# Kernel tuning notes

Measured on AMD Instinct MI355X. Metric: run time of the kernel, lower is better.

## Reference

```python
import jax, jax.numpy as jnp
import numpy as np

NUM_HEAD = 16
MASKED_BIAS = -10000.0


def setup_inputs() -> dict:
    key = jax.random.key(0)
    k1, k2, k3 = jax.random.split(key, 3)
    B, M, N = 2, 2048, 1024
    x = jax.random.normal(k1, (B, M, N), dtype=jnp.float32)
    w_attn = jax.random.normal(k2, (N, 3 * N), dtype=jnp.float32) * 0.02
    w_proj = jax.random.normal(k3, (N, N), dtype=jnp.float32) * 0.02
    b_attn = jnp.zeros((3 * N,), dtype=jnp.float32)
    b_proj = jnp.zeros((N,), dtype=jnp.float32)
    return {"x": x, "w_attn": w_attn, "w_proj": w_proj,
            "b_attn": b_attn, "b_proj": b_proj}


def reference(x, w_attn, w_proj, b_attn, b_proj):
    B, M, N = x.shape
    H = NUM_HEAD
    d = N // H  # head dim
    # fused QKV projection: [B,M,3N]
    qkv = jnp.einsum('bmn,nd->bmd', x, w_attn) + b_attn
    q, k, v = jnp.split(qkv, 3, axis=-1)
    # split heads -> [B,H,M,d]
    q = q.reshape(B, M, H, d).transpose(0, 2, 1, 3)
    k = k.reshape(B, M, H, d).transpose(0, 2, 1, 3)
    v = v.reshape(B, M, H, d).transpose(0, 2, 1, 3)
    # scaled dot-product scores [B,H,M,M]
    scores = jnp.einsum('bhqd,bhkd->bhqk', q, k) / jnp.sqrt(jnp.float32(d))
    causal = jnp.tril(jnp.ones((M, M), dtype=bool))  # GPT-2 bias buffer
    scores = jnp.where(causal, scores, jnp.float32(MASKED_BIAS))
    attn = jax.nn.softmax(scores, axis=-1)
    # context [B,H,M,d] -> [B,M,N]
    ctx = jnp.einsum('bhqk,bhkd->bhqd', attn, v)
    ctx = ctx.transpose(0, 2, 1, 3).reshape(B, M, N)
    # output projection
    out = jnp.einsum('bmn,no->bmo', ctx, w_proj) + b_proj
    return out
```

## Files before the change

### kernel.cpp

```cpp
#include <hip/hip_runtime.h>

typedef __attribute__((ext_vector_type(8))) __bf16 bf16x8;
typedef __attribute__((ext_vector_type(4))) __bf16 bf16x4;
typedef __attribute__((ext_vector_type(4))) float f32x4;
typedef __attribute__((ext_vector_type(4))) short short4v;

__device__ __forceinline__ void async_copy16(const void* g, void* l) {
    __builtin_amdgcn_global_load_lds(
        (const __attribute__((address_space(1))) void*)g,
        (__attribute__((address_space(3))) void*)l, 16, 0, 0);
}

__global__ __launch_bounds__(256) void prep_k(
    const float* __restrict__ x, __bf16* __restrict__ xb,
    const float* __restrict__ wa, __bf16* __restrict__ wAt,
    const float* __restrict__ wp, __bf16* __restrict__ wPt)
{
    __shared__ float tile[32][33];
    const int bx = blockIdx.x;
    if (bx < 2048) {
        size_t i = ((size_t)bx * 256 + threadIdx.x) * 8;
        float4 a = *(const float4*)&x[i];
        float4 b = *(const float4*)&x[i + 4];
        bf16x8 o;
        o[0] = (__bf16)a.x; o[1] = (__bf16)a.y; o[2] = (__bf16)a.z; o[3] = (__bf16)a.w;
        o[4] = (__bf16)b.x; o[5] = (__bf16)b.y; o[6] = (__bf16)b.z; o[7] = (__bf16)b.w;
        *(bf16x8*)&xb[i] = o;
        return;
    }
    const float* src; __bf16* dst; int R, C, c0, r0;
    if (bx < 5120) {
        int id = bx - 2048;
        src = wa; dst = wAt; R = 1024; C = 3072;
        c0 = (id % 96) * 32; r0 = (id / 96) * 32;
    } else {
        int id = bx - 5120;
        src = wp; dst = wPt; R = 1024; C = 1024;
        c0 = (id & 31) * 32; r0 = (id >> 5) * 32;
    }
    int tx = threadIdx.x & 31, ty = threadIdx.x >> 5;
    for (int i = ty; i < 32; i += 8)
        tile[i][tx] = src[(size_t)(r0 + i) * C + (c0 + tx)];
    __syncthreads();
    for (int i = ty; i < 32; i += 8)
        dst[(size_t)(c0 + i) * R + (r0 + tx)] = (__bf16)tile[tx][i];
}

template <int MODE, int TN>
__global__ __launch_bounds__(256) void gemm_bt(
    const __bf16* __restrict__ A, const __bf16* __restrict__ Bt,
    const float* __restrict__ bias, int K,
    __bf16* __restrict__ O0, __bf16* __restrict__ O1, __bf16* __restrict__ O2,
    float* __restrict__ Of)
{
    constexpr int NJ = TN / 32;
    __shared__ __align__(16) __bf16 lds_a[128 * 32];
    __shared__ __align__(16) __bf16 lds_b[TN * 32];
    const int row0 = blockIdx.x * 128;
    const int col0 = blockIdx.y * TN;
    const int tid  = threadIdx.x;
    const int lane = tid & 63;
    const int w    = tid >> 6;
    const int wm   = (w >> 1) * 64, wn = (w & 1) * (TN / 2);
    const int quad = lane >> 4, l16 = lane & 15;

    f32x4 acc[4][NJ] = {};
    for (int kb = 0; kb < K; kb += 32) {
#pragma unroll
        for (int t = 0; t < 2; ++t) {
            int s = t * 256 + tid;
            int L = s >> 3, c = (s & 7) ^ (L & 7);
            int row = 2 * L + (c >> 2), ch = c & 3;
            async_copy16(&A[(size_t)(row0 + row) * K + kb + ch * 8],
                         (char*)lds_a + (t * 256 + w * 64) * 16);
        }
#pragma unroll
        for (int t = 0; t < TN / 64; ++t) {
            int s = t * 256 + tid;
            int L = s >> 3, c = (s & 7) ^ (L & 7);
            int row = 2 * L + (c >> 2), ch = c & 3;
            async_copy16(&Bt[(size_t)(col0 + row) * K + kb + ch * 8],
                         (char*)lds_b + (t * 256 + w * 64) * 16);
        }
        __syncthreads();
        bf16x8 af[4], bfr[NJ];
#pragma unroll
        for (int i = 0; i < 4; ++i) {
            int r = wm + i * 16 + l16;
            int L = r >> 1, g = ((r & 1) * 4 + quad) ^ (L & 7);
            af[i] = *(const bf16x8*)&lds_a[L * 64 + g * 8];
        }
#pragma unroll
        for (int j = 0; j < NJ; ++j) {
            int r = wn + j * 16 + l16;
            int L = r >> 1, g = ((r & 1) * 4 + quad) ^ (L & 7);
            bfr[j] = *(const bf16x8*)&lds_b[L * 64 + g * 8];
        }
#pragma unroll
        for (int i = 0; i < 4; ++i)
#pragma unroll
            for (int j = 0; j < NJ; ++j)
                acc[i][j] = __builtin_amdgcn_mfma_f32_16x16x32_bf16(
                    af[i], bfr[j], acc[i][j], 0, 0, 0);
        __syncthreads();
    }

#pragma unroll
    for (int i = 0; i < 4; ++i) {
        int grow = row0 + wm + i * 16 + quad * 4;
#pragma unroll
        for (int j = 0; j < NJ; ++j) {
            int gcol = col0 + wn + j * 16 + l16;
            float bv = bias[gcol];
            if constexpr (MODE == 0) {
                int which = gcol >> 10;
                int n  = gcol & 1023;
                int hh = n >> 6, dd = n & 63;
                int bb = grow >> 11, mm0 = grow & 2047;
                int bhh = bb * 16 + hh;
                if (which == 2) {
                    int w64 = mm0 & 63;
                    int mi = (mm0 & ~63) | (w64 & 32) | ((w64 & 12) << 1)
                             | ((w64 & 16) >> 2);
                    bf16x4 pk;
#pragma unroll
                    for (int r = 0; r < 4; ++r)
                        pk[r] = (__bf16)(acc[i][j][r] + bv);
                    *(bf16x4*)&O2[((size_t)bhh * 64 + dd) * 2048 + mi] = pk;
                } else {
#pragma unroll
                    for (int r = 0; r < 4; ++r) {
                        float v = acc[i][j][r] + bv;
                        if (which == 0)
                            O0[((size_t)bhh * 2048 + mm0 + r) * 64 + dd] =
                                (__bf16)(v * 0.18033688011112042f);
                        else
                            O1[((size_t)bhh * 2048 + mm0 + r) * 64 + dd] =
                                (__bf16)v;
                    }
                }
            } else {
#pragma unroll
                for (int r = 0; r < 4; ++r) {
                    int gr = grow + r;
                    Of[(size_t)gr * 1024 + gcol] = acc[i][j][r] + bv;
                }
            }
        }
    }
}

__global__ __launch_bounds__(256) void attn_kernel(
    const __bf16* __restrict__ Qh, const __bf16* __restrict__ Kh,
    const __bf16* __restrict__ Vt, __bf16* __restrict__ ctx)
{
    const int M = 2048, D = 64;
    const int bh = blockIdx.x;
    const int qt = 31 - blockIdx.y;
    const int b = bh >> 4, h = bh & 15;
    const int tid = threadIdx.x, lane = tid & 63, w = tid >> 6;
    const int quad = lane >> 4, l16 = lane & 15;

    const int q0 = qt * 64;
    const int nIter = qt + 1;

    __shared__ __align__(16) __bf16 lds_k[2][64 * 64];
    __shared__ __align__(16) __bf16 lds_v[2][64 * 64];

    const __bf16* Qp = Qh + (size_t)bh * M * D;
    const __bf16* Kp = Kh + (size_t)bh * M * D;
    const __bf16* Vp = Vt + (size_t)bh * D * M;

    const int qw = q0 + w * 16;

    bf16x8 qf[2];
#pragma unroll
    for (int c = 0; c < 2; ++c)
        qf[c] = *(const bf16x8*)
            &Qp[(size_t)(qw + l16) * D + c * 32 + quad * 8];

    f32x4 acc2[4] = {};
    f32x4 acc_s = {};
    const short4v ones2 = {0x3F80, 0x3F80, 0x3F80, 0x3F80};

    auto stage = [&](int pb, int kb) {
#pragma unroll
        for (int t = 0; t < 2; ++t) {
            int c = w * 128 + t * 64 + lane;
            int row = c >> 3, ch = c & 7;
            int gch = ch ^ (row & 7);
            async_copy16(&Kp[(size_t)(kb + row) * 64 + gch * 8],
                         (char*)&lds_k[pb][0] + (w * 128 + t * 64) * 16);
            async_copy16(&Vp[(size_t)row * M + kb + gch * 8],
                         (char*)&lds_v[pb][0] + (w * 128 + t * 64) * 16);
        }
    };

    stage(0, 0);

    for (int it = 0; it < nIter; ++it) {
        const int kb = it << 6;
        __syncthreads();
        if (it + 1 < nIter) stage((it + 1) & 1, kb + 64);
        const __bf16* kt = &lds_k[it & 1][0];
        const __bf16* vt = &lds_v[it & 1][0];

        f32x4 s[4];
#pragma unroll
        for (int t = 0; t < 4; ++t) {
            f32x4 tt = {};
#pragma unroll
            for (int c = 0; c < 2; ++c) {
                int ch = ((c << 2) + quad) ^ (l16 & 7);
                bf16x8 kf = *(const bf16x8*)
                    &kt[(((t << 4) + l16) << 6) + (ch << 3)];
                tt = __builtin_amdgcn_mfma_f32_16x16x32_bf16(
                    kf, qf[c], tt, 0, 0, 0);
            }
            s[t] = tt;
        }
        if (kb + 63 > qw) {
#pragma unroll
            for (int t = 0; t < 4; ++t)
#pragma unroll
                for (int r = 0; r < 4; ++r)
                    if (kb + t * 16 + quad * 4 + r > qw + l16)
                        s[t][r] = -1e30f;
        }
        short4v pf[4];
#pragma unroll
        for (int t = 0; t < 4; ++t) {
            bf16x4 pk;
#pragma unroll
            for (int r = 0; r < 4; ++r)
                pk[r] = (__bf16)exp2f(s[t][r]);
            pf[t] = *(short4v*)&pk;
        }
#pragma unroll
        for (int f = 0; f < 4; ++f) {
            int row = (f << 4) + l16;
#pragma unroll
            for (int tp = 0; tp < 2; ++tp) {
                int g = ((tp << 2) + quad) ^ (row & 7);
                bf16x8 vv = *(const bf16x8*)&vt[(row << 6) + (g << 3)];
                bf16x4 lo = {vv[0], vv[1], vv[2], vv[3]};
                bf16x4 hi = {vv[4], vv[5], vv[6], vv[7]};
                acc2[f] = __builtin_amdgcn_mfma_f32_16x16x16bf16_1k(
                    *(short4v*)&lo, pf[2 * tp], acc2[f], 0, 0, 0);
                acc2[f] = __builtin_amdgcn_mfma_f32_16x16x16bf16_1k(
                    *(short4v*)&hi, pf[2 * tp + 1], acc2[f], 0, 0, 0);
            }
        }
#pragma unroll
        for (int t = 0; t < 4; ++t)
            acc_s = __builtin_amdgcn_mfma_f32_16x16x16bf16_1k(
                ones2, pf[t], acc_s, 0, 0, 0);
    }

    __syncthreads();
    __bf16* ldsT = &lds_k[0][0];
    const float l = acc_s[0];
#pragma unroll
    for (int f = 0; f < 4; ++f) {
        bf16x4 ov;
#pragma unroll
        for (int r = 0; r < 4; ++r)
            ov[r] = (__bf16)(acc2[f][r] / l);
        *(bf16x4*)&ldsT[(w * 16 + l16) * 72 + f * 16 + quad * 4] = ov;
    }
    __syncthreads();
    {
        int qq = tid >> 2;
        int dp = (tid & 3) * 16;
        const __bf16* src = &ldsT[qq * 72 + dp];
        __bf16* dst = &ctx[((size_t)(b * 2048 + q0 + qq)) * 1024 + h * 64 + dp];
        *(bf16x8*)&dst[0] = *(const bf16x8*)&src[0];
        *(bf16x8*)&dst[8] = *(const bf16x8*)&src[8];
    }
}

extern "C" void kernel_launch(void* const* d_in, const int* in_sizes, int n_in,
                              void* d_out, int out_size, void* d_ws, size_t ws_size,
                              hipStream_t stream) {
    const float* x      = (const float*)d_in[0];
    const float* w_attn = (const float*)d_in[1];
    const float* w_proj = (const float*)d_in[2];
    const float* b_attn = (const float*)d_in[3];
    const float* b_proj = (const float*)d_in[4];
    float* out = (float*)d_out;

    char* ws = (char*)d_ws;
    __bf16* xb  = (__bf16*)(ws);
    __bf16* ctx = (__bf16*)(ws);
    __bf16* wAt = (__bf16*)(ws + 8388608);
    __bf16* wPt = (__bf16*)(ws + 14680064);
    __bf16* Vt  = (__bf16*)(ws + 16777216);
    __bf16* Qh  = (__bf16*)d_out;
    __bf16* Kh  = (__bf16*)d_out + 4194304;

    prep_k<<<6144, 256, 0, stream>>>(x, xb, w_attn, wAt, w_proj, wPt);
    gemm_bt<0, 128><<<dim3(32, 24), 256, 0, stream>>>(xb, wAt, b_attn, 1024,
                                                      Qh, Kh, Vt, nullptr);
    attn_kernel<<<dim3(32, 32), 256, 0, stream>>>(Qh, Kh, Vt, ctx);
    gemm_bt<1, 64><<<dim3(32, 16), 256, 0, stream>>>(ctx, wPt, b_proj, 1024,
                                                     nullptr, nullptr, nullptr, out);
}
```

Baseline: 181.9 us.

## Enlarge attention query tile to 128 rows, two 16-row groups per wave

Each attention block now handles 128 query rows instead of 64, with each wave owning two 16-row query groups that share the same K/V fragments loaded from LDS. This halves the grid and halves the K/V global-to-LDS traffic per query row, and adds a per-wave skip of fully masked key tiles. The cost is more registers per thread (doubled accumulators and Q fragments), fewer blocks to balance the causal workload across CUs, and some waves idling on diagonal tiles.

```diff
diff --git a/kernel.cpp b/kernel.cpp
--- a/kernel.cpp
+++ b/kernel.cpp
@@ -156,13 +156,13 @@
 {
     const int M = 2048, D = 64;
     const int bh = blockIdx.x;
-    const int qt = 31 - blockIdx.y;
+    const int yt = 15 - blockIdx.y;
     const int b = bh >> 4, h = bh & 15;
     const int tid = threadIdx.x, lane = tid & 63, w = tid >> 6;
     const int quad = lane >> 4, l16 = lane & 15;
 
-    const int q0 = qt * 64;
-    const int nIter = qt + 1;
+    const int q0 = yt * 128;
+    const int nIter = 2 * yt + 2;
 
     __shared__ __align__(16) __bf16 lds_k[2][64 * 64];
     __shared__ __align__(16) __bf16 lds_v[2][64 * 64];
@@ -171,16 +171,18 @@
     const __bf16* Kp = Kh + (size_t)bh * M * D;
     const __bf16* Vp = Vt + (size_t)bh * D * M;
 
-    const int qw = q0 + w * 16;
-
-    bf16x8 qf[2];
-#pragma unroll
-    for (int c = 0; c < 2; ++c)
-        qf[c] = *(const bf16x8*)
-            &Qp[(size_t)(qw + l16) * D + c * 32 + quad * 8];
-
-    f32x4 acc2[4] = {};
-    f32x4 acc_s = {};
+    const int qw = q0 + w * 32;
+
+    bf16x8 qf[2][2];
+#pragma unroll
+    for (int g2 = 0; g2 < 2; ++g2)
+#pragma unroll
+        for (int c = 0; c < 2; ++c)
+            qf[g2][c] = *(const bf16x8*)
+                &Qp[(size_t)(qw + g2 * 16 + l16) * D + c * 32 + quad * 8];
+
+    f32x4 acc2[2][4] = {};
+    f32x4 acc_s[2] = {};
     const short4v ones2 = {0x3F80, 0x3F80, 0x3F80, 0x3F80};
 
     auto stage = [&](int pb, int kb) {
@@ -202,80 +204,95 @@
         const int kb = it << 6;
         __syncthreads();
         if (it + 1 < nIter) stage((it + 1) & 1, kb + 64);
+        if (kb > qw + 31) continue;
         const __bf16* kt = &lds_k[it & 1][0];
         const __bf16* vt = &lds_v[it & 1][0];
 
-        f32x4 s[4];
+        f32x4 s[2][4];
 #pragma unroll
         for (int t = 0; t < 4; ++t) {
-            f32x4 tt = {};
+            f32x4 t0 = {}, t1 = {};
 #pragma unroll
             for (int c = 0; c < 2; ++c) {
                 int ch = ((c << 2) + quad) ^ (l16 & 7);
                 bf16x8 kf = *(const bf16x8*)
                     &kt[(((t << 4) + l16) << 6) + (ch << 3)];
-                tt = __builtin_amdgcn_mfma_f32_16x16x32_bf16(
-                    kf, qf[c], tt, 0, 0, 0);
-            }
-            s[t] = tt;
-        }
-        if (kb + 63 > qw) {
+                t0 = __builtin_amdgcn_mfma_f32_16x16x32_bf16(
+                    kf, qf[0][c], t0, 0, 0, 0);
+                t1 = __builtin_amdgcn_mfma_f32_16x16x32_bf16(
+                    kf, qf[1][c], t1, 0, 0, 0);
+            }
+            s[0][t] = t0; s[1][t] = t1;
+        }
+#pragma unroll
+        for (int g2 = 0; g2 < 2; ++g2) {
+            int qg = qw + g2 * 16;
+            if (kb + 63 > qg) {
+#pragma unroll
+                for (int t = 0; t < 4; ++t)
+#pragma unroll
+                    for (int r = 0; r < 4; ++r)
+                        if (kb + t * 16 + quad * 4 + r > qg + l16)
+                            s[g2][t][r] = -1e30f;
+            }
+        }
+#pragma unroll
+        for (int g2 = 0; g2 < 2; ++g2) {
+            short4v pf[4];
+#pragma unroll
+            for (int t = 0; t < 4; ++t) {
+                bf16x4 pk;
+#pragma unroll
+                for (int r = 0; r < 4; ++r)
+                    pk[r] = (__bf16)exp2f(s[g2][t][r]);
+                pf[t] = *(short4v*)&pk;
+            }
+#pragma unroll
+            for (int f = 0; f < 4; ++f) {
+                int row = (f << 4) + l16;
+#pragma unroll
+                for (int tp = 0; tp < 2; ++tp) {
+                    int g = ((tp << 2) + quad) ^ (row & 7);
+                    bf16x8 vv = *(const bf16x8*)&vt[(row << 6) + (g << 3)];
+                    bf16x4 lo = {vv[0], vv[1], vv[2], vv[3]};
+                    bf16x4 hi = {vv[4], vv[5], vv[6], vv[7]};
+                    acc2[g2][f] = __builtin_amdgcn_mfma_f32_16x16x16bf16_1k(
+                        *(short4v*)&lo, pf[2 * tp], acc2[g2][f], 0, 0, 0);
+                    acc2[g2][f] = __builtin_amdgcn_mfma_f32_16x16x16bf16_1k(
+                        *(short4v*)&hi, pf[2 * tp + 1], acc2[g2][f], 0, 0, 0);
+                }
+            }
 #pragma unroll
             for (int t = 0; t < 4; ++t)
-#pragma unroll
-                for (int r = 0; r < 4; ++r)
-                    if (kb + t * 16 + quad * 4 + r > qw + l16)
-                        s[t][r] = -1e30f;
-        }
-        short4v pf[4];
-#pragma unroll
-        for (int t = 0; t < 4; ++t) {
-            bf16x4 pk;
-#pragma unroll
-            for (int r = 0; r < 4; ++r)
-                pk[r] = (__bf16)exp2f(s[t][r]);
-            pf[t] = *(short4v*)&pk;
-        }
-#pragma unroll
-        for (int f = 0; f < 4; ++f) {
-            int row = (f << 4) + l16;
-#pragma unroll
-            for (int tp = 0; tp < 2; ++tp) {
-                int g = ((tp << 2) + quad) ^ (row & 7);
-                bf16x8 vv = *(const bf16x8*)&vt[(row << 6) + (g << 3)];
-                bf16x4 lo = {vv[0], vv[1], vv[2], vv[3]};
-                bf16x4 hi = {vv[4], vv[5], vv[6], vv[7]};
-                acc2[f] = __builtin_amdgcn_mfma_f32_16x16x16bf16_1k(
-                    *(short4v*)&lo, pf[2 * tp], acc2[f], 0, 0, 0);
-                acc2[f] = __builtin_amdgcn_mfma_f32_16x16x16bf16_1k(
-                    *(short4v*)&hi, pf[2 * tp + 1], acc2[f], 0, 0, 0);
-            }
-        }
-#pragma unroll
-        for (int t = 0; t < 4; ++t)
-            acc_s = __builtin_amdgcn_mfma_f32_16x16x16bf16_1k(
-                ones2, pf[t], acc_s, 0, 0, 0);
+                acc_s[g2] = __builtin_amdgcn_mfma_f32_16x16x16bf16_1k(
+                    ones2, pf[t], acc_s[g2], 0, 0, 0);
+        }
     }
 
     __syncthreads();
     __bf16* ldsT = &lds_k[0][0];
-    const float l = acc_s[0];
-#pragma unroll
-    for (int f = 0; f < 4; ++f) {
-        bf16x4 ov;
-#pragma unroll
-        for (int r = 0; r < 4; ++r)
-            ov[r] = (__bf16)(acc2[f][r] / l);
-        *(bf16x4*)&ldsT[(w * 16 + l16) * 72 + f * 16 + quad * 4] = ov;
+#pragma unroll
+    for (int g2 = 0; g2 < 2; ++g2) {
+        const float l = acc_s[g2][0];
+#pragma unroll
+        for (int f = 0; f < 4; ++f) {
+            bf16x4 ov;
+#pragma unroll
+            for (int r = 0; r < 4; ++r)
+                ov[r] = (__bf16)(acc2[g2][f][r] / l);
+            *(bf16x4*)&ldsT[(w * 32 + g2 * 16 + l16) * 72 + f * 16 + quad * 4] = ov;
+        }
     }
     __syncthreads();
     {
-        int qq = tid >> 2;
-        int dp = (tid & 3) * 16;
+        int qq = tid >> 1;
+        int dp = (tid & 1) * 32;
         const __bf16* src = &ldsT[qq * 72 + dp];
         __bf16* dst = &ctx[((size_t)(b * 2048 + q0 + qq)) * 1024 + h * 64 + dp];
-        *(bf16x8*)&dst[0] = *(const bf16x8*)&src[0];
-        *(bf16x8*)&dst[8] = *(const bf16x8*)&src[8];
+        *(bf16x8*)&dst[0]  = *(const bf16x8*)&src[0];
+        *(bf16x8*)&dst[8]  = *(const bf16x8*)&src[8];
+        *(bf16x8*)&dst[16] = *(const bf16x8*)&src[16];
+        *(bf16x8*)&dst[24] = *(const bf16x8*)&src[24];
     }
 }
 
@@ -301,7 +318,7 @@
     prep_k<<<6144, 256, 0, stream>>>(x, xb, w_attn, wAt, w_proj, wPt);
     gemm_bt<0, 128><<<dim3(32, 24), 256, 0, stream>>>(xb, wAt, b_attn, 1024,
                                                       Qh, Kh, Vt, nullptr);
-    attn_kernel<<<dim3(32, 32), 256, 0, stream>>>(Qh, Kh, Vt, ctx);
+    attn_kernel<<<dim3(32, 16), 256, 0, stream>>>(Qh, Kh, Vt, ctx);
     gemm_bt<1, 64><<<dim3(32, 16), 256, 0, stream>>>(ctx, wPt, b_proj, 1024,
                                                      nullptr, nullptr, nullptr, out);
 }
```

New measurement: 196.4 us. 1.08x slower.
